# Optimization experiments

Hardware: AMD Instinct MI355X
Metric: run time of the kernel (lower is better)

Reference implementation:

```python
import jax, jax.numpy as jnp
import numpy as np
from jax import lax

B = 256
INPUT_DIM = 65536
SEQ = 128
VOCAB = INPUT_DIM // SEQ  # 512
LATENT = 128
HIDS = (1024, 512, 256)   # encoder hidden dims (hidden_dims[:-1])
ENC_OUT = 128             # hidden_dims[-1]
GRU_H = 128               # decoder hidden_dim = hidden_dims[-1]
BN_EPS = 1e-5
LRELU_SLOPE = 0.01


def setup_inputs() -> dict:
    key = jax.random.key(0)
    ks = iter(jax.random.split(key, 40))
    def w(shape, scale=0.02):
        return (jax.random.normal(next(ks), shape, dtype=jnp.float32) * scale)
    d = {}
    d['x'] = jax.random.normal(next(ks), (B, INPUT_DIM), dtype=jnp.float32)
    d['eps'] = jax.random.normal(next(ks), (B, LATENT), dtype=jnp.float32)
    dims = (INPUT_DIM,) + HIDS
    # encoder Linear+BN stacks
    for i in range(3):
        d[f'W{i}'] = w((dims[i + 1], dims[i]))
        d[f'b{i}'] = w((dims[i + 1],))
        d[f'g{i}'] = jnp.ones((dims[i + 1],), jnp.float32)
        d[f'be{i}'] = jnp.zeros((dims[i + 1],), jnp.float32)
    d['Wout'] = w((ENC_OUT, HIDS[-1]))
    d['bout'] = w((ENC_OUT,))
    d['Wmu'] = w((LATENT, ENC_OUT)); d['bmu'] = w((LATENT,))
    d['Wlv'] = w((LATENT, ENC_OUT)); d['blv'] = w((LATENT,))
    # GRU (num_layers=1), PyTorch gate order r,z,n
    d['Wih'] = w((3 * GRU_H, LATENT)); d['bih'] = w((3 * GRU_H,))
    d['Whh'] = w((3 * GRU_H, GRU_H)); d['bhh'] = w((3 * GRU_H,))
    d['Wfc'] = w((VOCAB, GRU_H)); d['bfc'] = w((VOCAB,))
    return d


def _bn(h, g, b):
    m = jnp.mean(h, axis=0)
    v = jnp.var(h, axis=0)
    return (h - m) * lax.rsqrt(v + BN_EPS) * g + b


def _lrelu(h):
    return jnp.where(h > 0, h, LRELU_SLOPE * h)


def reference(x, eps, W0, b0, g0, be0, W1, b1, g1, be1, W2, b2, g2, be2,
              Wout, bout, Wmu, bmu, Wlv, blv, Wih, bih, Whh, bhh, Wfc, bfc):
    # ---- encode ----
    h = x
    for W, b, g, be in ((W0, b0, g0, be0), (W1, b1, g1, be1), (W2, b2, g2, be2)):
        h = _lrelu(_bn(h @ W.T + b, g, be))
    h = h @ Wout.T + bout
    h1 = jax.nn.relu(h)
    mu = h1 @ Wmu.T + bmu
    logvar = h1 @ Wlv.T + blv
    # ---- reparameterize ----
    z = mu + eps * jnp.exp(0.5 * logvar)
    # ---- greedy decode: GRU step + argmax + one-hot, seq_length times ----
    # GRU input is the constant z each step -> precompute input projection once
    xp = z @ Wih.T + bih                       # [B, 3H]
    xr, xz, xn = jnp.split(xp, 3, axis=1)
    h0 = jnp.zeros((x.shape[0], GRU_H), x.dtype)

    def step(hid, _):
        hp = hid @ Whh.T + bhh
        hr, hz, hn = jnp.split(hp, 3, axis=1)
        r = jax.nn.sigmoid(xr + hr)
        zg = jax.nn.sigmoid(xz + hz)
        n = jnp.tanh(xn + r * hn)
        h2 = (1.0 - zg) * n + zg * hid
        logits = h2 @ Wfc.T + bfc              # [B, V]
        oh = jax.nn.one_hot(jnp.argmax(logits, axis=1), VOCAB, dtype=logits.dtype)
        return h2, oh

    _, outs = lax.scan(step, h0, None, length=SEQ)  # [S, B, V]
    out = jnp.transpose(outs, (1, 0, 2))            # [B, S, V]
    return out, mu, logvar
```

## Files before the change

kernel.cpp:

```cpp
#include <hip/hip_runtime.h>

#define DI __device__ __forceinline__

typedef __attribute__((ext_vector_type(8))) short s16x8;
typedef __attribute__((ext_vector_type(4))) float f32x4;

DI f32x4 mfma16(s16x8 a, s16x8 b, f32x4 c) {
  return __builtin_amdgcn_mfma_f32_16x16x32_bf16(a, b, c, 0, 0, 0);
}

DI unsigned short f2bf(float f) {
  unsigned int u = __builtin_bit_cast(unsigned int, f);
  u += 0x7fffu + ((u >> 16) & 1u);
  return (unsigned short)(u >> 16);
}
DI float bf2f(unsigned short h) {
  unsigned int u = ((unsigned int)h) << 16;
  return __builtin_bit_cast(float, u);
}
DI void split2(float f, unsigned short &hi, unsigned short &lo) {
  hi = f2bf(f);
  lo = f2bf(f - bf2f(hi));
}
DI void write_pair4(unsigned short* hp, unsigned short* lp, float4 v) {
  unsigned short h0,h1,h2,h3,l0,l1,l2,l3;
  split2(v.x,h0,l0); split2(v.y,h1,l1); split2(v.z,h2,l2); split2(v.w,h3,l3);
  *(ushort4*)hp = make_ushort4(h0,h1,h2,h3);
  *(ushort4*)lp = make_ushort4(l0,l1,l2,l3);
}

DI float fsig(float x)  { return __builtin_amdgcn_rcpf(1.f + __expf(-x)); }
DI float ftanhf(float x){ return 1.f - 2.f * __builtin_amdgcn_rcpf(1.f + __expf(2.f * x)); }

template<int M, int N, int K, int KS, bool SWZ>
__global__ __launch_bounds__(256, 2) void k_gemm(const float* __restrict__ A,
                                                 const float* __restrict__ Bw,
                                                 float* __restrict__ P) {
  constexpr int MT = M / 128, NT = N / 128;
  constexpr int KC = K / KS;
  constexpr int ITERS = KC / 32;
  int bid = blockIdx.x;
  int kidx, mt, nt;
  if (SWZ) {
    int xcd = bid & 7, s = bid >> 3;
    kidx = xcd + 8 * (s >> 4);
    int mn = s & 15; mt = mn >> 3; nt = mn & 7;
  } else {
    kidx = bid / (MT * NT);
    int mn = bid % (MT * NT);
    mt = mn / NT; nt = mn % NT;
  }
  int tid = threadIdx.x;
  int w = tid >> 6, lane = tid & 63, q = lane >> 4, l15 = lane & 15;
  int wm = w >> 1, wn = w & 1;

  __shared__ unsigned short Ah[2][4][128][8], Al[2][4][128][8];
  __shared__ unsigned short Bh[2][4][128][8], Bl[2][4][128][8];

  int srow = tid >> 1;
  int skb  = (tid & 1) * 16;
  const float* Abase = A  + (size_t)(mt * 128 + srow) * K + (size_t)kidx * KC;
  const float* Bbase = Bw + (size_t)(nt * 128 + srow) * K + (size_t)kidx * KC;

  float4 ra[4], rb[4];
  auto loadit = [&](int it) {
    const float* pa = Abase + it * 32 + skb;
    const float* pb = Bbase + it * 32 + skb;
#pragma unroll
    for (int i = 0; i < 4; i++) {
      ra[i] = *(const float4*)(pa + 4 * i);
      rb[i] = *(const float4*)(pb + 4 * i);
    }
  };
  auto stage = [&](int pb) {
#pragma unroll
    for (int i = 0; i < 4; i++) {
      int k0 = skb + 4 * i, qq = k0 >> 3, j0 = k0 & 7;
      write_pair4(&Ah[pb][qq][srow][j0], &Al[pb][qq][srow][j0], ra[i]);
      write_pair4(&Bh[pb][qq][srow][j0], &Bl[pb][qq][srow][j0], rb[i]);
    }
  };

  f32x4 acc[4][4];
#pragma unroll
  for (int i = 0; i < 4; i++)
#pragma unroll
    for (int j = 0; j < 4; j++) acc[i][j] = (f32x4){0.f, 0.f, 0.f, 0.f};

  loadit(0);
  stage(0);
  loadit(1);

  for (int it = 0; it < ITERS; ++it) {
    __syncthreads();
    if (it + 1 < ITERS) stage((it + 1) & 1);
    if (it + 2 < ITERS) loadit(it + 2);
    int pr = it & 1;

    s16x8 afh[4], afl[4], bfh[4], bfl[4];
#pragma unroll
    for (int t = 0; t < 4; t++) {
      int m = wm * 64 + 16 * t + l15;
      afh[t] = *(const s16x8*)&Ah[pr][q][m][0];
      afl[t] = *(const s16x8*)&Al[pr][q][m][0];
      int n = wn * 64 + 16 * t + l15;
      bfh[t] = *(const s16x8*)&Bh[pr][q][n][0];
      bfl[t] = *(const s16x8*)&Bl[pr][q][n][0];
    }
#pragma unroll
    for (int ti = 0; ti < 4; ti++)
#pragma unroll
      for (int tj = 0; tj < 4; tj++) {
        acc[ti][tj] = mfma16(afh[ti], bfh[tj], acc[ti][tj]);
        acc[ti][tj] = mfma16(afl[ti], bfh[tj], acc[ti][tj]);
        acc[ti][tj] = mfma16(afh[ti], bfl[tj], acc[ti][tj]);
      }
  }
#pragma unroll
  for (int ti = 0; ti < 4; ti++)
#pragma unroll
    for (int tj = 0; tj < 4; tj++)
#pragma unroll
      for (int r = 0; r < 4; r++) {
        int row = mt * 128 + wm * 64 + 16 * ti + 4 * q + r;
        int col = nt * 128 + wn * 64 + 16 * tj + l15;
        P[((size_t)kidx * M + row) * N + col] = acc[ti][tj][r];
      }
}

template<int KS>
__global__ __launch_bounds__(256) void k_red(const float* __restrict__ P,
                                             float* __restrict__ O) {
  int idx = blockIdx.x * 256 + threadIdx.x;
  float s = 0.f;
#pragma unroll
  for (int kk = 0; kk < KS; kk++) s += P[(size_t)kk * 262144 + idx];
  O[idx] = s;
}

template<int KS, int N>
__global__ __launch_bounds__(256) void k_bn(const float* __restrict__ P,
                                            const float* __restrict__ g,
                                            const float* __restrict__ be,
                                            float* __restrict__ a) {
  int tid = threadIdx.x;
  int c = tid & 15, bg = tid >> 4;
  int col = blockIdx.x * 16 + c;
  __shared__ float hbuf[256][16];
  __shared__ float sbuf[16][16], s2buf[16][16];
  __shared__ float msc[16], msh[16];
  float s = 0.f, s2 = 0.f;
  for (int b = bg * 16; b < bg * 16 + 16; b++) {
    float h = 0.f;
#pragma unroll
    for (int kk = 0; kk < KS; kk++) h += P[((size_t)kk * 256 + b) * N + col];
    hbuf[b][c] = h;
    s += h; s2 += h * h;
  }
  sbuf[bg][c] = s; s2buf[bg][c] = s2;
  __syncthreads();
  if (bg == 0) {
    float ts = 0.f, ts2 = 0.f;
#pragma unroll
    for (int i = 0; i < 16; i++) { ts += sbuf[i][c]; ts2 += s2buf[i][c]; }
    float m = ts * (1.f / 256.f);
    float v = ts2 * (1.f / 256.f) - m * m;
    float rs = rsqrtf(v + 1e-5f);
    float sc = g[col] * rs;
    msc[c] = sc;
    msh[c] = be[col] - m * sc;
  }
  __syncthreads();
  float sc = msc[c], sh = msh[c];
  for (int b = bg * 16; b < bg * 16 + 16; b++) {
    float v = hbuf[b][c] * sc + sh;
    a[(size_t)b * N + col] = v > 0.f ? v : 0.01f * v;
  }
}

__global__ __launch_bounds__(128) void k_head(const float* __restrict__ P3,
    const float* __restrict__ bout,
    const float* __restrict__ Wmu, const float* __restrict__ bmu,
    const float* __restrict__ Wlv, const float* __restrict__ blv,
    const float* __restrict__ Wih, const float* __restrict__ bih,
    const float* __restrict__ eps,
    float* __restrict__ out_mu, float* __restrict__ out_lv,
    float* __restrict__ xp) {
  int b = blockIdx.x, j = threadIdx.x;
  __shared__ float es[128], zs[128];
  float e = P3[(size_t)b * 128 + j] + P3[(size_t)(256 + b) * 128 + j] + bout[j];
  es[j] = e > 0.f ? e : 0.f;
  __syncthreads();
  float mu = bmu[j], lv = blv[j];
  for (int k = 0; k < 128; k++) {
    mu += es[k] * Wmu[j * 128 + k];
    lv += es[k] * Wlv[j * 128 + k];
  }
  out_mu[b * 128 + j] = mu;
  out_lv[b * 128 + j] = lv;
  float z = mu + eps[b * 128 + j] * expf(0.5f * lv);
  zs[j] = z;
  __syncthreads();
  for (int gi = 0; gi < 3; gi++) {
    int row = gi * 128 + j;
    float s = bih[row];
    for (int k = 0; k < 128; k++) s += zs[k] * Wih[row * 128 + k];
    xp[(size_t)b * 384 + row] = s;
  }
}

__global__ __launch_bounds__(256, 1) void k_gru(const float* __restrict__ Whh,
    const float* __restrict__ bhh, const float* __restrict__ xp,
    float* __restrict__ H) {
  int b0 = blockIdx.x * 16;
  int tid = threadIdx.x;
  int w = tid >> 6, lane = tid & 63, q = lane >> 4, l15 = lane & 15;
  __shared__ unsigned short h2hi[2][16][136], h2lo[2][16][136];
  __shared__ float hstage[9][16][132];
  (void)lane;

  int rb6[6];
  rb6[0] = 32 * w;        rb6[1] = 32 * w + 16;
  rb6[2] = 128 + 32 * w;  rb6[3] = 128 + 32 * w + 16;
  rb6[4] = 256 + 32 * w;  rb6[5] = 256 + 32 * w + 16;

  s16x8 wfh[6][4], wfl[6][4];
#pragma unroll
  for (int t = 0; t < 6; t++)
#pragma unroll
    for (int kt = 0; kt < 4; kt++) {
      const float* p = Whh + (size_t)(rb6[t] + l15) * 128 + kt * 32 + q * 8;
      s16x8 hi, lo;
#pragma unroll
      for (int j = 0; j < 8; j++) {
        unsigned short h, l; split2(p[j], h, l);
        hi[j] = (short)h; lo[j] = (short)l;
      }
      wfh[t][kt] = hi; wfl[t][kt] = lo;
    }

  int gb = b0 + l15;
  float xr_[2][4], xz_[2][4], xn_[2][4], bhn_[2][4], hprev[2][4];
#pragma unroll
  for (int t = 0; t < 2; t++)
#pragma unroll
    for (int r = 0; r < 4; r++) {
      int k0 = 32 * w + 16 * t + 4 * q + r;
      xr_[t][r] = xp[(size_t)gb * 384 + k0] + bhh[k0];
      xz_[t][r] = xp[(size_t)gb * 384 + 128 + k0] + bhh[128 + k0];
      xn_[t][r] = xp[(size_t)gb * 384 + 256 + k0];
      bhn_[t][r] = bhh[256 + k0];
      hprev[t][r] = 0.f;
    }

  for (int i = tid; i < 16 * 136; i += 256) {
    (&h2hi[0][0][0])[i] = 0;
    (&h2lo[0][0][0])[i] = 0;
  }
  __syncthreads();

  int hrow = tid >> 4, hcol = (tid & 15) * 8;
  int sl = 0;

  for (int s = 0; s < 128; s++) {
    int p = s & 1;
    s16x8 bhf[4], blf[4];
#pragma unroll
    for (int kt = 0; kt < 4; kt++) {
      bhf[kt] = *(const s16x8*)&h2hi[p][l15][kt * 32 + q * 8];
      blf[kt] = *(const s16x8*)&h2lo[p][l15][kt * 32 + q * 8];
    }
    if ((s & 7) == 0 && s) {
      int fb = s - 8;
#pragma unroll
      for (int ss = 0; ss < 8; ss++) {
        int t9 = sl + 1 + ss;
        int fsl = t9 >= 9 ? t9 - 9 : t9;
        float4 v0 = *(const float4*)&hstage[fsl][hrow][hcol];
        float4 v1 = *(const float4*)&hstage[fsl][hrow][hcol + 4];
        float* dst = H + ((size_t)(b0 + hrow) * 128 + fb + ss) * 128 + hcol;
        *(float4*)dst = v0;
        *(float4*)(dst + 4) = v1;
      }
    }

    f32x4 accm[6], accc[6];
#pragma unroll
    for (int t = 0; t < 6; t++) {
      accm[t] = (f32x4){0.f, 0.f, 0.f, 0.f};
      accc[t] = (f32x4){0.f, 0.f, 0.f, 0.f};
    }
    const int ord[6] = {0, 2, 4, 1, 3, 5};
#pragma unroll
    for (int oi = 0; oi < 6; oi++) {
      int t = ord[oi];
#pragma unroll
      for (int kt = 0; kt < 4; kt++) {
        accm[t] = mfma16(wfh[t][kt], bhf[kt], accm[t]);
        accc[t] = mfma16(wfl[t][kt], bhf[kt], accc[t]);
        accc[t] = mfma16(wfh[t][kt], blf[kt], accc[t]);
      }
    }

#pragma unroll
    for (int t = 0; t < 2; t++) {
      unsigned short hs[4], ls[4];
      float hv[4];
#pragma unroll
      for (int r = 0; r < 4; r++) {
        float hr = accm[t][r] + accc[t][r];
        float hz = accm[2 + t][r] + accc[2 + t][r];
        float hn = accm[4 + t][r] + accc[4 + t][r];
        float rg = fsig(xr_[t][r] + hr);
        float zg = fsig(xz_[t][r] + hz);
        float ng = ftanhf(fmaf(rg, hn + bhn_[t][r], xn_[t][r]));
        float h2 = fmaf(zg, hprev[t][r] - ng, ng);
        hprev[t][r] = h2;
        hv[r] = h2;
        split2(h2, hs[r], ls[r]);
      }
      int kb = 32 * w + 16 * t + 4 * q;
      *(float4*)&hstage[sl][l15][kb] = make_float4(hv[0], hv[1], hv[2], hv[3]);
      *(ushort4*)&h2hi[p ^ 1][l15][kb] = make_ushort4(hs[0], hs[1], hs[2], hs[3]);
      *(ushort4*)&h2lo[p ^ 1][l15][kb] = make_ushort4(ls[0], ls[1], ls[2], ls[3]);
    }
    sl = (sl == 8) ? 0 : sl + 1;
    __syncthreads();
  }
#pragma unroll
  for (int ss = 0; ss < 8; ss++) {
    int fb = 120 + ss;
    int fsl = fb % 9;
    float4 v0 = *(const float4*)&hstage[fsl][hrow][hcol];
    float4 v1 = *(const float4*)&hstage[fsl][hrow][hcol + 4];
    float* dst = H + ((size_t)(b0 + hrow) * 128 + fb) * 128 + hcol;
    *(float4*)dst = v0;
    *(float4*)(dst + 4) = v1;
  }
}

__global__ __launch_bounds__(256, 2) void k_fc(const float* __restrict__ H,
    const float* __restrict__ Wfc, const float* __restrict__ bfc,
    float* __restrict__ out) {
  int rows0 = blockIdx.x * 64;
  int tid = threadIdx.x;
  int w = tid >> 6, lane = tid & 63, q = lane >> 4, l15 = lane & 15;
  __shared__ unsigned short Ah[4][4][64][8], Al[4][4][64][8];
  __shared__ unsigned short Bh[4][4][32][8], Bl[4][4][32][8];
  __shared__ int argbuf[64];
  (void)lane;

  {
    int row = tid >> 2, kb = (tid & 3) * 32;
    const float* p = H + (size_t)(rows0 + row) * 128 + kb;
#pragma unroll
    for (int i = 0; i < 8; i++) {
      float4 v = *(const float4*)(p + 4 * i);
      int k0 = kb + 4 * i;
      int kt = k0 >> 5, qq = (k0 >> 3) & 3, j0 = k0 & 7;
      write_pair4(&Ah[kt][qq][row][j0], &Al[kt][qq][row][j0], v);
    }
  }
  __syncthreads();

  s16x8 afh[4], afl[4];
#pragma unroll
  for (int kt = 0; kt < 4; kt++) {
    afh[kt] = *(const s16x8*)&Ah[kt][q][16 * w + l15][0];
    afl[kt] = *(const s16x8*)&Al[kt][q][16 * w + l15][0];
  }

  float best[4]; int bidx[4];
#pragma unroll
  for (int r = 0; r < 4; r++) { best[r] = -3.4e38f; bidx[r] = 0; }

  for (int c = 0; c < 16; c++) {
    {
      int n = tid >> 3, kb = (tid & 7) * 16;
      const float* p = Wfc + (size_t)(c * 32 + n) * 128 + kb;
#pragma unroll
      for (int i = 0; i < 4; i++) {
        float4 v = *(const float4*)(p + 4 * i);
        int k0 = kb + 4 * i;
        int kt = k0 >> 5, qq = (k0 >> 3) & 3, j0 = k0 & 7;
        write_pair4(&Bh[kt][qq][n][j0], &Bl[kt][qq][n][j0], v);
      }
    }
    __syncthreads();
    f32x4 acc[2];
    acc[0] = (f32x4){0.f, 0.f, 0.f, 0.f};
    acc[1] = (f32x4){0.f, 0.f, 0.f, 0.f};
#pragma unroll
    for (int nt = 0; nt < 2; nt++)
#pragma unroll
      for (int kt = 0; kt < 4; kt++) {
        s16x8 bh = *(const s16x8*)&Bh[kt][q][nt * 16 + l15][0];
        s16x8 bl = *(const s16x8*)&Bl[kt][q][nt * 16 + l15][0];
        acc[nt] = mfma16(afh[kt], bh, acc[nt]);
        acc[nt] = mfma16(afl[kt], bh, acc[nt]);
        acc[nt] = mfma16(afh[kt], bl, acc[nt]);
      }
#pragma unroll
    for (int nt = 0; nt < 2; nt++)
#pragma unroll
      for (int r = 0; r < 4; r++) {
        int col = c * 32 + nt * 16 + l15;
        float v = acc[nt][r] + bfc[col];
        if (v > best[r]) { best[r] = v; bidx[r] = col; }
      }
    __syncthreads();
  }

#pragma unroll
  for (int r = 0; r < 4; r++) {
    float bv = best[r]; int bi = bidx[r];
    for (int off = 8; off >= 1; off >>= 1) {
      float ov = __shfl_xor(bv, off, 64);
      int oi = __shfl_xor(bi, off, 64);
      if (ov > bv || (ov == bv && oi < bi)) { bv = ov; bi = oi; }
    }
    if (l15 == 0) argbuf[16 * w + 4 * q + r] = bi;
  }
  __syncthreads();

  int row = tid >> 2, cb = (tid & 3) * 128;
  int am = argbuf[row];
  float* op = out + (size_t)(rows0 + row) * 512 + cb;
#pragma unroll
  for (int i = 0; i < 32; i++) {
    float4 v = {0.f, 0.f, 0.f, 0.f};
    int base = cb + 4 * i;
    if (am >= base && am < base + 4) ((float*)&v)[am - base] = 1.0f;
    *(float4*)(op + 4 * i) = v;
  }
}

extern "C" void kernel_launch(void* const* d_in, const int* in_sizes, int n_in,
                              void* d_out, int out_size, void* d_ws, size_t ws_size,
                              hipStream_t stream) {
  const float* x    = (const float*)d_in[0];
  const float* eps  = (const float*)d_in[1];
  const float* W0   = (const float*)d_in[2];
  const float* g0   = (const float*)d_in[4];
  const float* be0  = (const float*)d_in[5];
  const float* W1   = (const float*)d_in[6];
  const float* g1   = (const float*)d_in[8];
  const float* be1  = (const float*)d_in[9];
  const float* W2   = (const float*)d_in[10];
  const float* g2   = (const float*)d_in[12];
  const float* be2  = (const float*)d_in[13];
  const float* Wout = (const float*)d_in[14];
  const float* bout = (const float*)d_in[15];
  const float* Wmu  = (const float*)d_in[16];
  const float* bmu  = (const float*)d_in[17];
  const float* Wlv  = (const float*)d_in[18];
  const float* blv  = (const float*)d_in[19];
  const float* Wih  = (const float*)d_in[20];
  const float* bih  = (const float*)d_in[21];
  const float* Whh  = (const float*)d_in[22];
  const float* bhh  = (const float*)d_in[23];
  const float* Wfc  = (const float*)d_in[24];
  const float* bfc  = (const float*)d_in[25];

  float* out    = (float*)d_out;
  float* mu_out = out + 16777216;
  float* lv_out = out + 16777216 + 32768;

  const bool big = ws_size >= 75900000ull;
  const int KS0 = big ? 64 : 16;

  float* ws  = (float*)d_ws;
  float* P0  = ws;
  float* O0  = ws + (size_t)262144 * KS0;
  float* a1  = O0 + 262144;
  float* P1  = a1 + 262144;
  float* a2  = P1 + 1048576;
  float* P2  = a2 + 131072;
  float* a3  = P2 + 262144;
  float* P3  = a3 + 65536;
  float* xp  = P3 + 65536;
  float* Hst = ws;

  if (big) {
    hipLaunchKernelGGL((k_gemm<256,1024,65536,64,true>), dim3(1024), dim3(256), 0, stream, x, W0, P0);
    hipLaunchKernelGGL((k_red<64>),                      dim3(1024), dim3(256), 0, stream, P0, O0);
  } else {
    hipLaunchKernelGGL((k_gemm<256,1024,65536,16,true>), dim3(256),  dim3(256), 0, stream, x, W0, P0);
    hipLaunchKernelGGL((k_red<16>),                      dim3(1024), dim3(256), 0, stream, P0, O0);
  }
  hipLaunchKernelGGL((k_bn<1,1024>),                   dim3(64),  dim3(256), 0, stream, O0, g0, be0, a1);
  hipLaunchKernelGGL((k_gemm<256,512,1024,8,false>),   dim3(64),  dim3(256), 0, stream, a1, W1, P1);
  hipLaunchKernelGGL((k_bn<8,512>),                    dim3(32),  dim3(256), 0, stream, P1, g1, be1, a2);
  hipLaunchKernelGGL((k_gemm<256,256,512,4,false>),    dim3(16),  dim3(256), 0, stream, a2, W2, P2);
  hipLaunchKernelGGL((k_bn<4,256>),                    dim3(16),  dim3(256), 0, stream, P2, g2, be2, a3);
  hipLaunchKernelGGL((k_gemm<256,128,256,2,false>),    dim3(4),   dim3(256), 0, stream, a3, Wout, P3);
  hipLaunchKernelGGL(k_head, dim3(256), dim3(128), 0, stream, P3, bout, Wmu, bmu, Wlv, blv, Wih, bih, eps, mu_out, lv_out, xp);
  hipLaunchKernelGGL(k_gru,  dim3(16),  dim3(256), 0, stream, Whh, bhh, xp, Hst);
  hipLaunchKernelGGL(k_fc,   dim3(512), dim3(256), 0, stream, Hst, Wfc, bfc, out);
}
```

Before: 884.5 us.

## Use packed bf16 conversion, reorder MFMAs, widen GRU block to 512 threads

```diff
diff --git a/kernel.cpp b/kernel.cpp
--- a/kernel.cpp
+++ b/kernel.cpp
@@ -22,11 +22,26 @@
   hi = f2bf(f);
   lo = f2bf(f - bf2f(hi));
 }
-DI void write_pair4(unsigned short* hp, unsigned short* lp, float4 v) {
-  unsigned short h0,h1,h2,h3,l0,l1,l2,l3;
-  split2(v.x,h0,l0); split2(v.y,h1,l1); split2(v.z,h2,l2); split2(v.w,h3,l3);
-  *(ushort4*)hp = make_ushort4(h0,h1,h2,h3);
-  *(ushort4*)lp = make_ushort4(l0,l1,l2,l3);
+
+DI unsigned int cvtpk(float a, float b) {
+  unsigned int r;
+  asm("v_cvt_pk_bf16_f32 %0, %1, %2" : "=v"(r) : "v"(a), "v"(b));
+  return r;
+}
+DI float fromlo(unsigned int u) { return __builtin_bit_cast(float, u << 16); }
+DI float fromhi(unsigned int u) { return __builtin_bit_cast(float, u & 0xffff0000u); }
+
+DI void write_pair8(unsigned short* hp, unsigned short* lp, float4 a, float4 b) {
+  unsigned int h01 = cvtpk(a.x, a.y), h23 = cvtpk(a.z, a.w);
+  unsigned int h45 = cvtpk(b.x, b.y), h67 = cvtpk(b.z, b.w);
+  unsigned int l01 = cvtpk(a.x - fromlo(h01), a.y - fromhi(h01));
+  unsigned int l23 = cvtpk(a.z - fromlo(h23), a.w - fromhi(h23));
+  unsigned int l45 = cvtpk(b.x - fromlo(h45), b.y - fromhi(h45));
+  unsigned int l67 = cvtpk(b.z - fromlo(h67), b.w - fromhi(h67));
+  uint4 H4; H4.x = h01; H4.y = h23; H4.z = h45; H4.w = h67;
+  uint4 L4; L4.x = l01; L4.y = l23; L4.z = l45; L4.w = l67;
+  *(uint4*)hp = H4;
+  *(uint4*)lp = L4;
 }
 
 DI float fsig(float x)  { return __builtin_amdgcn_rcpf(1.f + __expf(-x)); }
@@ -73,12 +88,11 @@
     }
   };
   auto stage = [&](int pb) {
-#pragma unroll
-    for (int i = 0; i < 4; i++) {
-      int k0 = skb + 4 * i, qq = k0 >> 3, j0 = k0 & 7;
-      write_pair4(&Ah[pb][qq][srow][j0], &Al[pb][qq][srow][j0], ra[i]);
-      write_pair4(&Bh[pb][qq][srow][j0], &Bl[pb][qq][srow][j0], rb[i]);
-    }
+    int qq0 = skb >> 3;
+    write_pair8(&Ah[pb][qq0][srow][0],     &Al[pb][qq0][srow][0],     ra[0], ra[1]);
+    write_pair8(&Ah[pb][qq0 + 1][srow][0], &Al[pb][qq0 + 1][srow][0], ra[2], ra[3]);
+    write_pair8(&Bh[pb][qq0][srow][0],     &Bl[pb][qq0][srow][0],     rb[0], rb[1]);
+    write_pair8(&Bh[pb][qq0 + 1][srow][0], &Bl[pb][qq0 + 1][srow][0], rb[2], rb[3]);
   };
 
   f32x4 acc[4][4];
@@ -110,11 +124,18 @@
 #pragma unroll
     for (int ti = 0; ti < 4; ti++)
 #pragma unroll
-      for (int tj = 0; tj < 4; tj++) {
+      for (int tj = 0; tj < 4; tj++)
         acc[ti][tj] = mfma16(afh[ti], bfh[tj], acc[ti][tj]);
+#pragma unroll
+    for (int ti = 0; ti < 4; ti++)
+#pragma unroll
+      for (int tj = 0; tj < 4; tj++)
         acc[ti][tj] = mfma16(afl[ti], bfh[tj], acc[ti][tj]);
+#pragma unroll
+    for (int ti = 0; ti < 4; ti++)
+#pragma unroll
+      for (int tj = 0; tj < 4; tj++)
         acc[ti][tj] = mfma16(afh[ti], bfl[tj], acc[ti][tj]);
-      }
   }
 #pragma unroll
   for (int ti = 0; ti < 4; ti++)
@@ -209,7 +230,7 @@
   }
 }
 
-__global__ __launch_bounds__(256, 1) void k_gru(const float* __restrict__ Whh,
+__global__ __launch_bounds__(512, 2) void k_gru(const float* __restrict__ Whh,
     const float* __restrict__ bhh, const float* __restrict__ xp,
     float* __restrict__ H) {
   int b0 = blockIdx.x * 16;
@@ -219,17 +240,17 @@
   __shared__ float hstage[9][16][132];
   (void)lane;
 
-  int rb6[6];
-  rb6[0] = 32 * w;        rb6[1] = 32 * w + 16;
-  rb6[2] = 128 + 32 * w;  rb6[3] = 128 + 32 * w + 16;
-  rb6[4] = 256 + 32 * w;  rb6[5] = 256 + 32 * w + 16;
-
-  s16x8 wfh[6][4], wfl[6][4];
-#pragma unroll
-  for (int t = 0; t < 6; t++)
+  int rb3[3];
+  rb3[0] = 16 * w;
+  rb3[1] = 128 + 16 * w;
+  rb3[2] = 256 + 16 * w;
+
+  s16x8 wfh[3][4], wfl[3][4];
+#pragma unroll
+  for (int t = 0; t < 3; t++)
 #pragma unroll
     for (int kt = 0; kt < 4; kt++) {
-      const float* p = Whh + (size_t)(rb6[t] + l15) * 128 + kt * 32 + q * 8;
+      const float* p = Whh + (size_t)(rb3[t] + l15) * 128 + kt * 32 + q * 8;
       s16x8 hi, lo;
 #pragma unroll
       for (int j = 0; j < 8; j++) {
@@ -240,26 +261,25 @@
     }
 
   int gb = b0 + l15;
-  float xr_[2][4], xz_[2][4], xn_[2][4], bhn_[2][4], hprev[2][4];
-#pragma unroll
-  for (int t = 0; t < 2; t++)
-#pragma unroll
-    for (int r = 0; r < 4; r++) {
-      int k0 = 32 * w + 16 * t + 4 * q + r;
-      xr_[t][r] = xp[(size_t)gb * 384 + k0] + bhh[k0];
-      xz_[t][r] = xp[(size_t)gb * 384 + 128 + k0] + bhh[128 + k0];
-      xn_[t][r] = xp[(size_t)gb * 384 + 256 + k0];
-      bhn_[t][r] = bhh[256 + k0];
-      hprev[t][r] = 0.f;
-    }
-
-  for (int i = tid; i < 16 * 136; i += 256) {
+  int k0 = 16 * w + 4 * q;
+  float xr_[4], xz_[4], xn_[4], bhn_[4], hprev[4];
+#pragma unroll
+  for (int r = 0; r < 4; r++) {
+    int kk = k0 + r;
+    xr_[r] = xp[(size_t)gb * 384 + kk] + bhh[kk];
+    xz_[r] = xp[(size_t)gb * 384 + 128 + kk] + bhh[128 + kk];
+    xn_[r] = xp[(size_t)gb * 384 + 256 + kk];
+    bhn_[r] = bhh[256 + kk];
+    hprev[r] = 0.f;
+  }
+
+  for (int i = tid; i < 16 * 136; i += 512) {
     (&h2hi[0][0][0])[i] = 0;
     (&h2lo[0][0][0])[i] = 0;
   }
   __syncthreads();
 
-  int hrow = tid >> 4, hcol = (tid & 15) * 8;
+  int hrow = tid >> 5, hcol = (tid & 31) * 4;
   int sl = 0;
 
   for (int s = 0; s < 128; s++) {
@@ -276,54 +296,48 @@
       for (int ss = 0; ss < 8; ss++) {
         int t9 = sl + 1 + ss;
         int fsl = t9 >= 9 ? t9 - 9 : t9;
-        float4 v0 = *(const float4*)&hstage[fsl][hrow][hcol];
-        float4 v1 = *(const float4*)&hstage[fsl][hrow][hcol + 4];
-        float* dst = H + ((size_t)(b0 + hrow) * 128 + fb + ss) * 128 + hcol;
-        *(float4*)dst = v0;
-        *(float4*)(dst + 4) = v1;
+        float4 v = *(const float4*)&hstage[fsl][hrow][hcol];
+        *(float4*)(H + ((size_t)(b0 + hrow) * 128 + fb + ss) * 128 + hcol) = v;
       }
     }
 
-    f32x4 accm[6], accc[6];
-#pragma unroll
-    for (int t = 0; t < 6; t++) {
+    f32x4 accm[3], accc[3];
+#pragma unroll
+    for (int t = 0; t < 3; t++) {
       accm[t] = (f32x4){0.f, 0.f, 0.f, 0.f};
       accc[t] = (f32x4){0.f, 0.f, 0.f, 0.f};
     }
-    const int ord[6] = {0, 2, 4, 1, 3, 5};
-#pragma unroll
-    for (int oi = 0; oi < 6; oi++) {
-      int t = ord[oi];
-#pragma unroll
-      for (int kt = 0; kt < 4; kt++) {
-        accm[t] = mfma16(wfh[t][kt], bhf[kt], accm[t]);
-        accc[t] = mfma16(wfl[t][kt], bhf[kt], accc[t]);
-        accc[t] = mfma16(wfh[t][kt], blf[kt], accc[t]);
-      }
-    }
-
-#pragma unroll
-    for (int t = 0; t < 2; t++) {
-      unsigned short hs[4], ls[4];
-      float hv[4];
-#pragma unroll
-      for (int r = 0; r < 4; r++) {
-        float hr = accm[t][r] + accc[t][r];
-        float hz = accm[2 + t][r] + accc[2 + t][r];
-        float hn = accm[4 + t][r] + accc[4 + t][r];
-        float rg = fsig(xr_[t][r] + hr);
-        float zg = fsig(xz_[t][r] + hz);
-        float ng = ftanhf(fmaf(rg, hn + bhn_[t][r], xn_[t][r]));
-        float h2 = fmaf(zg, hprev[t][r] - ng, ng);
-        hprev[t][r] = h2;
-        hv[r] = h2;
-        split2(h2, hs[r], ls[r]);
-      }
-      int kb = 32 * w + 16 * t + 4 * q;
-      *(float4*)&hstage[sl][l15][kb] = make_float4(hv[0], hv[1], hv[2], hv[3]);
-      *(ushort4*)&h2hi[p ^ 1][l15][kb] = make_ushort4(hs[0], hs[1], hs[2], hs[3]);
-      *(ushort4*)&h2lo[p ^ 1][l15][kb] = make_ushort4(ls[0], ls[1], ls[2], ls[3]);
-    }
+#pragma unroll
+    for (int kt = 0; kt < 4; kt++) {
+#pragma unroll
+      for (int t = 0; t < 3; t++) accm[t] = mfma16(wfh[t][kt], bhf[kt], accm[t]);
+#pragma unroll
+      for (int t = 0; t < 3; t++) accc[t] = mfma16(wfl[t][kt], bhf[kt], accc[t]);
+#pragma unroll
+      for (int t = 0; t < 3; t++) accc[t] = mfma16(wfh[t][kt], blf[kt], accc[t]);
+    }
+
+    float hv[4];
+#pragma unroll
+    for (int r = 0; r < 4; r++) {
+      float hr = accm[0][r] + accc[0][r];
+      float hz = accm[1][r] + accc[1][r];
+      float hn = accm[2][r] + accc[2][r];
+      float rg = fsig(xr_[r] + hr);
+      float zg = fsig(xz_[r] + hz);
+      float ng = ftanhf(fmaf(rg, hn + bhn_[r], xn_[r]));
+      float h2 = fmaf(zg, hprev[r] - ng, ng);
+      hprev[r] = h2;
+      hv[r] = h2;
+    }
+    unsigned int h01 = cvtpk(hv[0], hv[1]), h23 = cvtpk(hv[2], hv[3]);
+    unsigned int l01 = cvtpk(hv[0] - fromlo(h01), hv[1] - fromhi(h01));
+    unsigned int l23 = cvtpk(hv[2] - fromlo(h23), hv[3] - fromhi(h23));
+    *(float4*)&hstage[sl][l15][k0] = make_float4(hv[0], hv[1], hv[2], hv[3]);
+    uint2 hh; hh.x = h01; hh.y = h23;
+    uint2 ll; ll.x = l01; ll.y = l23;
+    *(uint2*)&h2hi[p ^ 1][l15][k0] = hh;
+    *(uint2*)&h2lo[p ^ 1][l15][k0] = ll;
     sl = (sl == 8) ? 0 : sl + 1;
     __syncthreads();
   }
@@ -331,11 +345,8 @@
   for (int ss = 0; ss < 8; ss++) {
     int fb = 120 + ss;
     int fsl = fb % 9;
-    float4 v0 = *(const float4*)&hstage[fsl][hrow][hcol];
-    float4 v1 = *(const float4*)&hstage[fsl][hrow][hcol + 4];
-    float* dst = H + ((size_t)(b0 + hrow) * 128 + fb) * 128 + hcol;
-    *(float4*)dst = v0;
-    *(float4*)(dst + 4) = v1;
+    float4 v = *(const float4*)&hstage[fsl][hrow][hcol];
+    *(float4*)(H + ((size_t)(b0 + hrow) * 128 + fb) * 128 + hcol) = v;
   }
 }
 
@@ -353,13 +364,13 @@
   {
     int row = tid >> 2, kb = (tid & 3) * 32;
     const float* p = H + (size_t)(rows0 + row) * 128 + kb;
-#pragma unroll
-    for (int i = 0; i < 8; i++) {
-      float4 v = *(const float4*)(p + 4 * i);
-      int k0 = kb + 4 * i;
-      int kt = k0 >> 5, qq = (k0 >> 3) & 3, j0 = k0 & 7;
-      write_pair4(&Ah[kt][qq][row][j0], &Al[kt][qq][row][j0], v);
-    }
+    int kt = kb >> 5;
+    float4 v[8];
+#pragma unroll
+    for (int i = 0; i < 8; i++) v[i] = *(const float4*)(p + 4 * i);
+#pragma unroll
+    for (int j = 0; j < 4; j++)
+      write_pair8(&Ah[kt][j][row][0], &Al[kt][j][row][0], v[2 * j], v[2 * j + 1]);
   }
   __syncthreads();
 
@@ -378,27 +389,33 @@
     {
       int n = tid >> 3, kb = (tid & 7) * 16;
       const float* p = Wfc + (size_t)(c * 32 + n) * 128 + kb;
-#pragma unroll
-      for (int i = 0; i < 4; i++) {
-        float4 v = *(const float4*)(p + 4 * i);
-        int k0 = kb + 4 * i;
-        int kt = k0 >> 5, qq = (k0 >> 3) & 3, j0 = k0 & 7;
-        write_pair4(&Bh[kt][qq][n][j0], &Bl[kt][qq][n][j0], v);
-      }
+      int kt = kb >> 5, qq0 = (kb >> 3) & 3;
+      float4 v0 = *(const float4*)(p);
+      float4 v1 = *(const float4*)(p + 4);
+      float4 v2 = *(const float4*)(p + 8);
+      float4 v3 = *(const float4*)(p + 12);
+      write_pair8(&Bh[kt][qq0][n][0],     &Bl[kt][qq0][n][0],     v0, v1);
+      write_pair8(&Bh[kt][qq0 + 1][n][0], &Bl[kt][qq0 + 1][n][0], v2, v3);
     }
     __syncthreads();
     f32x4 acc[2];
     acc[0] = (f32x4){0.f, 0.f, 0.f, 0.f};
     acc[1] = (f32x4){0.f, 0.f, 0.f, 0.f};
+    s16x8 bh[2][4], bl[2][4];
 #pragma unroll
     for (int nt = 0; nt < 2; nt++)
 #pragma unroll
       for (int kt = 0; kt < 4; kt++) {
-        s16x8 bh = *(const s16x8*)&Bh[kt][q][nt * 16 + l15][0];
-        s16x8 bl = *(const s16x8*)&Bl[kt][q][nt * 16 + l15][0];
-        acc[nt] = mfma16(afh[kt], bh, acc[nt]);
-        acc[nt] = mfma16(afl[kt], bh, acc[nt]);
-        acc[nt] = mfma16(afh[kt], bl, acc[nt]);
+        bh[nt][kt] = *(const s16x8*)&Bh[kt][q][nt * 16 + l15][0];
+        bl[nt][kt] = *(const s16x8*)&Bl[kt][q][nt * 16 + l15][0];
+      }
+#pragma unroll
+    for (int kt = 0; kt < 4; kt++)
+#pragma unroll
+      for (int nt = 0; nt < 2; nt++) {
+        acc[nt] = mfma16(afh[kt], bh[nt][kt], acc[nt]);
+        acc[nt] = mfma16(afl[kt], bh[nt][kt], acc[nt]);
+        acc[nt] = mfma16(afh[kt], bl[nt][kt], acc[nt]);
       }
 #pragma unroll
     for (int nt = 0; nt < 2; nt++)
@@ -495,6 +512,6 @@
   hipLaunchKernelGGL((k_bn<4,256>),                    dim3(16),  dim3(256), 0, stream, P2, g2, be2, a3);
   hipLaunchKernelGGL((k_gemm<256,128,256,2,false>),    dim3(4),   dim3(256), 0, stream, a3, Wout, P3);
   hipLaunchKernelGGL(k_head, dim3(256), dim3(128), 0, stream, P3, bout, Wmu, bmu, Wlv, blv, Wih, bih, eps, mu_out, lv_out, xp);
-  hipLaunchKernelGGL(k_gru,  dim3(16),  dim3(256), 0, stream, Whh, bhh, xp, Hst);
+  hipLaunchKernelGGL(k_gru,  dim3(16),  dim3(512), 0, stream, Whh, bhh, xp, Hst);
   hipLaunchKernelGGL(k_fc,   dim3(512), dim3(256), 0, stream, Hst, Wfc, bfc, out);
 }
```

Measured after the change: 785.5 us. 1.13x faster.
